# Performance work log

Measured on AMD Instinct MI355X. Metric: run time of the kernel, lower is better.

The kernel has to match this reference:

```python
import jax, jax.numpy as jnp
import numpy as np

TOKEN_ATTEND_SELF_VALUE = -0.0005
LN_EPS = 1e-5


def _layer_norm(x, g, b):
    mu = jnp.mean(x, axis=-1, keepdims=True)
    var = jnp.mean(jnp.square(x - mu), axis=-1, keepdims=True)
    return (x - mu) * jax.lax.rsqrt(var + LN_EPS) * g + b


def _gelu(x):
    return jax.nn.gelu(x, approximate=False)  # torch nn.GELU default is exact erf


def _grouped_ff(x, w1, b1, w2, b2):
    # x: [b, n, L, d]; per-level (grouped conv1d k=1) feedforward
    h = _gelu(jnp.einsum('bnld,ldm->bnlm', x, w1) + b1)
    return _gelu(jnp.einsum('bnlm,lmd->bnld', h, w2) + b2)


def _consensus_attention(levels):
    # levels: [b, n, L, d]; attend_self=False, no local mask
    b, n, L, d = levels.shape
    norm = jnp.maximum(jnp.linalg.norm(levels, axis=-1, keepdims=True), 1e-12)
    k = levels / norm  # F.normalize(dim=-1)
    sim = jnp.einsum('bild,bjld->blij', levels, k) * (d ** -0.5)
    eye = jnp.eye(n, dtype=bool)[None, None, :, :]
    sim = jnp.where(eye, TOKEN_ATTEND_SELF_VALUE, sim)
    attn = jax.nn.softmax(sim, axis=-1)
    return jnp.einsum('blij,bjld->bild', attn, levels)


def setup_inputs() -> dict:
    key = jax.random.key(0)
    ks = jax.random.split(key, 12)
    B, C, H, W = 2, 3, 48, 48
    dim, L = 32, 5
    n = H * W  # sub_patch_size = 1
    s = 0.02
    inp = {
        'img': jax.random.normal(ks[0], (B, C, H, W), jnp.float32),
        'w_tok': jax.random.normal(ks[1], (C, dim), jnp.float32) * s,
        'b_tok': jnp.zeros((dim,), jnp.float32),
        'g_ln_tok': jnp.ones((dim,), jnp.float32),
        'b_ln_tok': jnp.zeros((dim,), jnp.float32),
        'w_lvl': jax.random.normal(ks[2], (C, L * dim), jnp.float32) * s,
        'b_lvl': jnp.zeros((L * dim,), jnp.float32),
        'g_ln_lvl': jnp.ones((dim,), jnp.float32),
        'b_ln_lvl': jnp.zeros((dim,), jnp.float32),
        'pos_emb': jax.random.normal(ks[3], (n, dim), jnp.float32) * s,
        'bu_w1': jax.random.normal(ks[4], (L, dim, 4 * dim), jnp.float32) * s,
        'bu_b1': jnp.zeros((L, 4 * dim), jnp.float32),
        'bu_w2': jax.random.normal(ks[5], (L, 4 * dim, dim), jnp.float32) * s,
        'bu_b2': jnp.zeros((L, dim), jnp.float32),
        'td_w1': jax.random.normal(ks[6], (L - 1, dim, 4 * dim), jnp.float32) * s,
        'td_b1': jnp.zeros((L - 1, 4 * dim), jnp.float32),
        'td_w2': jax.random.normal(ks[7], (L - 1, 4 * dim, dim), jnp.float32) * s,
        'td_b2': jnp.zeros((L - 1, dim), jnp.float32),
        'iters': 3,
    }
    return inp


def reference(img, w_tok, b_tok, g_ln_tok, b_ln_tok, w_lvl, b_lvl, g_ln_lvl,
              b_ln_lvl, pos_emb, bu_w1, bu_b1, bu_w2, bu_b2, td_w1, td_b1,
              td_w2, td_b2, iters):
    B, C, H, W = img.shape
    L = bu_w1.shape[0]
    dim = w_tok.shape[1]
    x = jnp.transpose(img, (0, 2, 3, 1)).reshape(B, H * W, C)  # b n c

    # image_to_tokens: Linear -> LayerNorm -> GELU
    tokens = _gelu(_layer_norm(x @ w_tok + b_tok, g_ln_tok, b_ln_tok))  # [b,n,d]

    # image_to_levels: 1x1 Conv -> GELU -> reshape -> LayerNorm
    lv = _gelu(x @ w_lvl + b_lvl).reshape(B, H * W, L, dim)
    levels = _layer_norm(lv, g_ln_lvl, b_ln_lvl)  # [b,n,L,d]

    pos = pos_emb[None, :, None, :]  # () n () d
    bottom = tokens[:, :, None, :]  # [b,n,1,d]

    num_contrib = jnp.array([4.0] * (L - 1) + [3.0], jnp.float32)[None, None, :, None]

    for _ in range(iters):
        lwi = jnp.concatenate([bottom, levels], axis=2)  # [b,n,L+1,d]
        bu = _grouped_ff(lwi[:, :, :-1, :], bu_w1, bu_b1, bu_w2, bu_b2)
        td = _grouped_ff(lwi[:, :, 2:, :] + pos, td_w1, td_b1, td_w2, td_b2)
        td = jnp.pad(td, ((0, 0), (0, 0), (0, 1), (0, 0)))  # zero at top level
        cons = _consensus_attention(levels)
        levels = (levels + bu + td + cons) / num_contrib

    return levels
```

## Files before the change

kernel.cpp:

```cpp
#include <hip/hip_runtime.h>
#include <math.h>

#define BB 2
#define NN 2304
#define DIM 32
#define LL 5
#define HID 128
#define SJ 8
#define BLN (BB * LL * NN)
#define CONSGRID (SJ * 18 * LL * BB)
#define FFGRID (9 * 36)
#define COMBGRID (BLN / 32)

#define QK_SCALE2 0.25503486f
#define SELF_VAL2 (-7.2134752e-4f)

typedef __attribute__((ext_vector_type(8))) short bf16x8;
typedef __attribute__((ext_vector_type(16))) float f32x16;

union B8U { bf16x8 v; unsigned u[4]; };

__device__ __forceinline__ float b2f(unsigned bits16) {
    union { float f; unsigned u; } c; c.u = bits16 << 16; return c.f;
}
__device__ __forceinline__ unsigned cvt_pk_bf16(float lo, float hi) {
    unsigned r;
    asm("v_cvt_pk_bf16_f32 %0, %1, %2" : "=v"(r) : "v"(lo), "v"(hi));
    return r;
}
__device__ __forceinline__ float gelu_f(float v) {
    return 0.5f * v * (1.0f + erff(v * 0.70710678118654752f));
}
__device__ __forceinline__ void plswap(unsigned a, unsigned b, unsigned& o0, unsigned& o1) {
    auto r = __builtin_amdgcn_permlane32_swap(a, b, false, false);
    o0 = r[0]; o1 = r[1];
}

__global__ __launch_bounds__(256) void prep_all(
    const float* __restrict__ img,
    const float* __restrict__ w_tok, const float* __restrict__ b_tok,
    const float* __restrict__ g_ln_tok, const float* __restrict__ b_ln_tok,
    const float* __restrict__ w_lvl, const float* __restrict__ b_lvl,
    const float* __restrict__ g_ln_lvl, const float* __restrict__ b_ln_lvl,
    const float* __restrict__ pos_emb,
    const float* __restrict__ bu_w1, const float* __restrict__ bu_w2,
    const float* __restrict__ td_w1, const float* __restrict__ td_w2,
    float* __restrict__ levels, short* __restrict__ tokensB,
    short* __restrict__ Qb, short* __restrict__ Ksb, short* __restrict__ Vtb,
    short* __restrict__ TDb, short* __restrict__ W1T, short* __restrict__ W2T)
{
    int blk = blockIdx.x, tid = threadIdx.x;
    int rq = tid >> 2, q = tid & 3, d0 = q * 8;
    if (blk < 72) {
        int t = blk * 64 + rq;
        int b = t / NN, i = t - b * NN;
        float x0 = img[(size_t)(b * 3 + 0) * NN + i];
        float x1 = img[(size_t)(b * 3 + 1) * NN + i];
        float x2 = img[(size_t)(b * 3 + 2) * NN + i];
        float v[8];
        float red = 0.f;
        #pragma unroll
        for (int m = 0; m < 8; ++m) {
            int c = d0 + m;
            v[m] = x0 * w_tok[c] + x1 * w_tok[DIM + c] + x2 * w_tok[2 * DIM + c] + b_tok[c];
            red += v[m];
        }
        red += __shfl_xor(red, 1, 64);
        red += __shfl_xor(red, 2, 64);
        float mu = red * (1.0f / DIM);
        float vr = 0.f;
        #pragma unroll
        for (int m = 0; m < 8; ++m) { float dd = v[m] - mu; vr += dd * dd; }
        vr += __shfl_xor(vr, 1, 64);
        vr += __shfl_xor(vr, 2, 64);
        float rs = rsqrtf(vr * (1.0f / DIM) + 1e-5f);
        unsigned tw[4];
        #pragma unroll
        for (int d2 = 0; d2 < 4; ++d2) {
            int c = d0 + 2 * d2;
            float ya = gelu_f((v[2 * d2] - mu) * rs * g_ln_tok[c] + b_ln_tok[c]);
            float yb = gelu_f((v[2 * d2 + 1] - mu) * rs * g_ln_tok[c + 1] + b_ln_tok[c + 1]);
            tw[d2] = cvt_pk_bf16(ya, yb);
        }
        *(uint4*)(tokensB + (size_t)t * DIM + d0) = make_uint4(tw[0], tw[1], tw[2], tw[3]);
    } else if (blk < 432) {
        int z = blk - 72;
        int b = z / 180, rem = z % 180;
        int l = rem / 36, ic = rem % 36;
        int i = ic * 64 + rq;
        int t = b * NN + i;
        float x0 = img[(size_t)(b * 3 + 0) * NN + i];
        float x1 = img[(size_t)(b * 3 + 1) * NN + i];
        float x2 = img[(size_t)(b * 3 + 2) * NN + i];
        float u[8];
        float red = 0.f;
        #pragma unroll
        for (int m = 0; m < 8; ++m) {
            int c = l * DIM + d0 + m;
            float pre = x0 * w_lvl[c] + x1 * w_lvl[LL * DIM + c] + x2 * w_lvl[2 * LL * DIM + c] + b_lvl[c];
            u[m] = gelu_f(pre);
            red += u[m];
        }
        red += __shfl_xor(red, 1, 64);
        red += __shfl_xor(red, 2, 64);
        float mu = red * (1.0f / DIM);
        float vr = 0.f;
        #pragma unroll
        for (int m = 0; m < 8; ++m) { float dd = u[m] - mu; vr += dd * dd; }
        vr += __shfl_xor(vr, 1, 64);
        vr += __shfl_xor(vr, 2, 64);
        float rs = rsqrtf(vr * (1.0f / DIM) + 1e-5f);
        float y[8];
        float n2p = 0.f;
        #pragma unroll
        for (int m = 0; m < 8; ++m) {
            int c = d0 + m;
            y[m] = (u[m] - mu) * rs * g_ln_lvl[c] + b_ln_lvl[c];
            n2p += y[m] * y[m];
        }
        n2p += __shfl_xor(n2p, 1, 64);
        n2p += __shfl_xor(n2p, 2, 64);
        float ksc = QK_SCALE2 / fmaxf(sqrtf(n2p), 1e-12f);
        size_t lo = ((size_t)t * LL + l) * DIM + d0;
        *(float4*)(levels + lo)     = make_float4(y[0], y[1], y[2], y[3]);
        *(float4*)(levels + lo + 4) = make_float4(y[4], y[5], y[6], y[7]);
        size_t qro = ((size_t)(b * LL + l) * NN + i) * DIM + d0;
        unsigned qw[4], kw[4];
        #pragma unroll
        for (int d2 = 0; d2 < 4; ++d2) {
            qw[d2] = cvt_pk_bf16(y[2 * d2], y[2 * d2 + 1]);
            kw[d2] = cvt_pk_bf16(y[2 * d2] * ksc, y[2 * d2 + 1] * ksc);
        }
        *(uint4*)(Qb + qro)  = make_uint4(qw[0], qw[1], qw[2], qw[3]);
        *(uint4*)(Ksb + qro) = make_uint4(kw[0], kw[1], kw[2], kw[3]);
        #pragma unroll
        for (int d2 = 0; d2 < 4; ++d2) {
            unsigned uv = cvt_pk_bf16(y[2 * d2], y[2 * d2 + 1]);
            Vtb[((size_t)(b * LL + l) * DIM + d0 + 2 * d2) * NN + i]     = (short)uv;
            Vtb[((size_t)(b * LL + l) * DIM + d0 + 2 * d2 + 1) * NN + i] = (short)(uv >> 16);
        }
        if (l >= 1) {
            unsigned dw[4];
            #pragma unroll
            for (int d2 = 0; d2 < 4; ++d2) {
                float p0 = pos_emb[(size_t)i * DIM + d0 + 2 * d2];
                float p1 = pos_emb[(size_t)i * DIM + d0 + 2 * d2 + 1];
                dw[d2] = cvt_pk_bf16(y[2 * d2] + p0, y[2 * d2 + 1] + p1);
            }
            *(uint4*)(TDb + ((size_t)(b * 4 + (l - 1)) * NN + i) * DIM + d0) =
                make_uint4(dw[0], dw[1], dw[2], dw[3]);
        }
    } else {
        int g = blk - 432;
        bool is_bu = g < LL;
        int lw = is_bu ? g : g - LL;
        const float* W1 = (is_bu ? bu_w1 : td_w1) + (size_t)lw * DIM * HID;
        const float* W2 = (is_bu ? bu_w2 : td_w2) + (size_t)lw * HID * DIM;
        short* o1 = W1T + (size_t)g * HID * DIM;
        short* o2 = W2T + (size_t)g * DIM * HID;
        for (int e = tid; e < HID * DIM; e += 256) {
            int m = e >> 5, d = e & 31;
            unsigned u1 = cvt_pk_bf16(W1[(size_t)d * HID + m], 0.f);
            o1[e] = (short)u1;
            int dd = e >> 7, mm = e & 127;
            unsigned u2 = cvt_pk_bf16(W2[(size_t)mm * DIM + dd], 0.f);
            o2[e] = (short)u2;
        }
    }
}

__global__ __launch_bounds__(256) void cons_ff(
    const short* __restrict__ Qb, const short* __restrict__ Ksb,
    const short* __restrict__ Vtb,
    const short* __restrict__ tokensB, const short* __restrict__ TDb,
    const short* __restrict__ W1T, const short* __restrict__ W2T,
    const float* __restrict__ bu_b1, const float* __restrict__ bu_b2,
    const float* __restrict__ td_b1, const float* __restrict__ td_b2,
    short* __restrict__ accp, float* __restrict__ sump,
    float* __restrict__ bu_out, float* __restrict__ td_out)
{
    __shared__ float b1_lds[HID];
    __shared__ float b2_lds[DIM];
    __shared__ __align__(16) float yt_lds[4][DIM * 32];

    int tid = threadIdx.x;
    int w = tid >> 6, lane = tid & 63;
    int li = lane & 31, hi = lane >> 5;

    if (blockIdx.x < CONSGRID) {
        int bid = blockIdx.x;
        int s = bid % SJ; int rest = bid / SJ;
        int ibig = rest % 18; rest /= 18;
        int l = rest % 5, b = rest / 5;
        int i0 = ibig * 128 + w * 32;

        const short* Qrow = Qb + (size_t)(b * LL + l) * NN * DIM;
        const short* Krow = Ksb + (size_t)(b * LL + l) * NN * DIM;
        const short* Vrow = Vtb + (size_t)(b * LL + l) * DIM * NN;

        bf16x8 qf0 = *(const bf16x8*)(Qrow + (size_t)(i0 + li) * DIM + hi * 8);
        bf16x8 qf1 = *(const bf16x8*)(Qrow + (size_t)(i0 + li) * DIM + 16 + hi * 8);

        f32x16 outacc = {};
        float ssum = 0.f;

        for (int jt = 0; jt < NN / SJ / 32; ++jt) {
            int j0 = s * (NN / SJ) + jt * 32;
            bf16x8 kf0 = *(const bf16x8*)(Krow + (size_t)(j0 + li) * DIM + hi * 8);
            bf16x8 kf1 = *(const bf16x8*)(Krow + (size_t)(j0 + li) * DIM + 16 + hi * 8);
            f32x16 st = {};
            st = __builtin_amdgcn_mfma_f32_32x32x16_bf16(kf0, qf0, st, 0, 0, 0);
            st = __builtin_amdgcn_mfma_f32_32x32x16_bf16(kf1, qf1, st, 0, 0, 0);
            float e[16];
            if (j0 == i0) {
                #pragma unroll
                for (int r = 0; r < 16; ++r) {
                    float sc = st[r];
                    if ((((r & 3) + 8 * (r >> 2) + 4 * hi) == li)) sc = SELF_VAL2;
                    e[r] = exp2f(sc);
                }
            } else {
                #pragma unroll
                for (int r = 0; r < 16; ++r) e[r] = exp2f(st[r]);
            }
            #pragma unroll
            for (int r = 0; r < 16; ++r) ssum += e[r];
            unsigned wpk[8];
            #pragma unroll
            for (int h2 = 0; h2 < 8; ++h2)
                wpk[h2] = cvt_pk_bf16(e[2 * h2], e[2 * h2 + 1]);
            B8U pa0, pa1;
            plswap(wpk[0], wpk[2], pa0.u[0], pa0.u[2]);
            plswap(wpk[1], wpk[3], pa0.u[1], pa0.u[3]);
            plswap(wpk[4], wpk[6], pa1.u[0], pa1.u[2]);
            plswap(wpk[5], wpk[7], pa1.u[1], pa1.u[3]);
            bf16x8 vf0 = *(const bf16x8*)(Vrow + (size_t)li * NN + j0 + hi * 8);
            bf16x8 vf1 = *(const bf16x8*)(Vrow + (size_t)li * NN + j0 + 16 + hi * 8);
            outacc = __builtin_amdgcn_mfma_f32_32x32x16_bf16(pa0.v, vf0, outacc, 0, 0, 0);
            outacc = __builtin_amdgcn_mfma_f32_32x32x16_bf16(pa1.v, vf1, outacc, 0, 0, 0);
        }
        size_t base = (size_t)s * BLN + (size_t)(b * LL + l) * NN;
        float ss2 = ssum + __shfl_xor(ssum, 32, 64);
        if (lane < 32) sump[base + i0 + li] = ss2;
        #pragma unroll
        for (int r = 0; r < 16; r += 2) {
            unsigned uo = cvt_pk_bf16(outacc[r], outacc[r + 1]);
            int il = (r & 3) + 8 * (r >> 2) + 4 * hi;
            accp[(base + i0 + il) * DIM + li]     = (short)uo;
            accp[(base + i0 + il + 1) * DIM + li] = (short)(uo >> 16);
        }
    } else {
        int fb = blockIdx.x - CONSGRID;
        int g = fb / 36;
        int tile = fb % 36;

        bool is_bu = g < LL;
        int lw = is_bu ? g : g - LL;
        const float* B1 = (is_bu ? bu_b1 : td_b1) + (size_t)lw * HID;
        const float* B2 = (is_bu ? bu_b2 : td_b2) + (size_t)lw * DIM;
        if (tid < HID) b1_lds[tid] = B1[tid];
        if (tid < DIM) b2_lds[tid] = B2[tid];
        __syncthreads();

        int t0 = tile * 128 + w * 32;
        int b = t0 / NN;
        int i0 = t0 - b * NN;
        const short* xrow =
            (g == 0) ? (tokensB + (size_t)t0 * DIM)
          : is_bu    ? (Qb + ((size_t)(b * LL + (g - 1)) * NN + i0) * DIM)
                     : (TDb + ((size_t)(b * 4 + (g - LL)) * NN + i0) * DIM);
        const short* w1g = W1T + (size_t)g * HID * DIM;
        const short* w2g = W2T + (size_t)g * DIM * HID;

        bf16x8 xb0 = *(const bf16x8*)(xrow + (size_t)li * DIM + hi * 8);
        bf16x8 xb1 = *(const bf16x8*)(xrow + (size_t)li * DIM + 16 + hi * 8);

        f32x16 yacc = {};
        #pragma unroll
        for (int ht = 0; ht < 4; ++ht) {
            bf16x8 a0 = *(const bf16x8*)(w1g + (size_t)(ht * 32 + li) * DIM + hi * 8);
            bf16x8 a1 = *(const bf16x8*)(w1g + (size_t)(ht * 32 + li) * DIM + 16 + hi * 8);
            f32x16 hT = {};
            hT = __builtin_amdgcn_mfma_f32_32x32x16_bf16(a0, xb0, hT, 0, 0, 0);
            hT = __builtin_amdgcn_mfma_f32_32x32x16_bf16(a1, xb1, hT, 0, 0, 0);
            float h[16];
            #pragma unroll
            for (int r = 0; r < 16; ++r) {
                int lrow = (r & 3) + 8 * (r >> 2) + 4 * hi;
                h[r] = gelu_f(hT[r] + b1_lds[ht * 32 + lrow]);
            }
            unsigned wp[8];
            #pragma unroll
            for (int h2 = 0; h2 < 8; ++h2)
                wp[h2] = cvt_pk_bf16(h[2 * h2], h[2 * h2 + 1]);
            B8U hb0, hb1;
            plswap(wp[0], wp[2], hb0.u[0], hb0.u[2]);
            plswap(wp[1], wp[3], hb0.u[1], hb0.u[3]);
            plswap(wp[4], wp[6], hb1.u[0], hb1.u[2]);
            plswap(wp[5], wp[7], hb1.u[1], hb1.u[3]);
            bf16x8 a2 = *(const bf16x8*)(w2g + (size_t)li * HID + ht * 32 + hi * 8);
            bf16x8 a3 = *(const bf16x8*)(w2g + (size_t)li * HID + ht * 32 + 16 + hi * 8);
            yacc = __builtin_amdgcn_mfma_f32_32x32x16_bf16(a2, hb0.v, yacc, 0, 0, 0);
            yacc = __builtin_amdgcn_mfma_f32_32x32x16_bf16(a3, hb1.v, yacc, 0, 0, 0);
        }
        float* yt = yt_lds[w];
        #pragma unroll
        for (int r = 0; r < 16; ++r) {
            int dr = (r & 3) + 8 * (r >> 2) + 4 * hi;
            yt[dr * 32 + li] = gelu_f(yacc[r] + b2_lds[dr]);
        }
        int tk = lane >> 1, dh = (lane & 1) * 16;
        float ov[16];
        #pragma unroll
        for (int j = 0; j < 16; ++j) ov[j] = yt[(dh + j) * 32 + tk];
        float* op = (is_bu ? bu_out : td_out) + ((size_t)(t0 + tk) * LL + lw) * DIM + dh;
        #pragma unroll
        for (int j4 = 0; j4 < 4; ++j4)
            ((float4*)op)[j4] = make_float4(ov[4 * j4], ov[4 * j4 + 1], ov[4 * j4 + 2], ov[4 * j4 + 3]);
    }
}

__global__ __launch_bounds__(256) void combine8(
    const float* __restrict__ levels, const float* __restrict__ bu_buf,
    const float* __restrict__ td_buf, const float* __restrict__ pos_emb,
    const short* __restrict__ accp, const float* __restrict__ sump,
    float* __restrict__ levels_next,
    short* __restrict__ Qb, short* __restrict__ Ksb, short* __restrict__ Vtb,
    short* __restrict__ TDb)
{
    int rw = blockIdx.x * 32 + (threadIdx.x >> 3);
    int dq = threadIdx.x & 7;
    int d0 = dq * 4;
    int b = rw / (LL * NN);
    int l = (rw / NN) % LL;
    int i = rw % NN;
    size_t ro = (size_t)rw;

    float ssum = 0.f;
    #pragma unroll
    for (int s = 0; s < SJ; ++s) ssum += sump[(size_t)s * BLN + ro];
    float inv_s = 1.0f / ssum;
    float nc = (l == LL - 1) ? (1.0f / 3.0f) : 0.25f;

    float ax[4] = {0.f, 0.f, 0.f, 0.f};
    #pragma unroll
    for (int s = 0; s < SJ; ++s) {
        uint2 av = *(const uint2*)(accp + ((size_t)s * BLN + ro) * DIM + d0);
        ax[0] += b2f(av.x & 0xFFFFu);
        ax[1] += b2f(av.x >> 16);
        ax[2] += b2f(av.y & 0xFFFFu);
        ax[3] += b2f(av.y >> 16);
    }

    size_t lo = ((size_t)(b * NN + i) * LL + l) * DIM + d0;
    float4 lv = *(const float4*)(levels + lo);
    float4 bu = *(const float4*)(bu_buf + lo);
    float4 td = (l < LL - 1) ? *(const float4*)(td_buf + lo) : make_float4(0.f, 0.f, 0.f, 0.f);

    float o[4];
    o[0] = (lv.x + bu.x + td.x + ax[0] * inv_s) * nc;
    o[1] = (lv.y + bu.y + td.y + ax[1] * inv_s) * nc;
    o[2] = (lv.z + bu.z + td.z + ax[2] * inv_s) * nc;
    o[3] = (lv.w + bu.w + td.w + ax[3] * inv_s) * nc;
    *(float4*)(levels_next + lo) = make_float4(o[0], o[1], o[2], o[3]);

    float n2p = o[0] * o[0] + o[1] * o[1] + o[2] * o[2] + o[3] * o[3];
    n2p += __shfl_xor(n2p, 1, 64);
    n2p += __shfl_xor(n2p, 2, 64);
    n2p += __shfl_xor(n2p, 4, 64);
    float ksc = QK_SCALE2 / fmaxf(sqrtf(n2p), 1e-12f);

    size_t qro = ro * DIM + d0;
    unsigned q0 = cvt_pk_bf16(o[0], o[1]);
    unsigned q1 = cvt_pk_bf16(o[2], o[3]);
    unsigned k0 = cvt_pk_bf16(o[0] * ksc, o[1] * ksc);
    unsigned k1 = cvt_pk_bf16(o[2] * ksc, o[3] * ksc);
    *(uint2*)(Qb + qro)  = make_uint2(q0, q1);
    *(uint2*)(Ksb + qro) = make_uint2(k0, k1);
    Vtb[((size_t)(b * LL + l) * DIM + d0 + 0) * NN + i] = (short)q0;
    Vtb[((size_t)(b * LL + l) * DIM + d0 + 1) * NN + i] = (short)(q0 >> 16);
    Vtb[((size_t)(b * LL + l) * DIM + d0 + 2) * NN + i] = (short)q1;
    Vtb[((size_t)(b * LL + l) * DIM + d0 + 3) * NN + i] = (short)(q1 >> 16);
    if (l >= 1) {
        float p0 = pos_emb[(size_t)i * DIM + d0 + 0];
        float p1 = pos_emb[(size_t)i * DIM + d0 + 1];
        float p2 = pos_emb[(size_t)i * DIM + d0 + 2];
        float p3 = pos_emb[(size_t)i * DIM + d0 + 3];
        unsigned t0 = cvt_pk_bf16(o[0] + p0, o[1] + p1);
        unsigned t1 = cvt_pk_bf16(o[2] + p2, o[3] + p3);
        *(uint2*)(TDb + ((size_t)(b * 4 + (l - 1)) * NN + i) * DIM + d0) = make_uint2(t0, t1);
    }
}

extern "C" void kernel_launch(void* const* d_in, const int* in_sizes, int n_in,
                              void* d_out, int out_size, void* d_ws, size_t ws_size,
                              hipStream_t stream)
{
    (void)in_sizes; (void)n_in; (void)out_size; (void)ws_size;
    const float* img      = (const float*)d_in[0];
    const float* w_tok    = (const float*)d_in[1];
    const float* b_tok    = (const float*)d_in[2];
    const float* g_ln_tok = (const float*)d_in[3];
    const float* b_ln_tok = (const float*)d_in[4];
    const float* w_lvl    = (const float*)d_in[5];
    const float* b_lvl    = (const float*)d_in[6];
    const float* g_ln_lvl = (const float*)d_in[7];
    const float* b_ln_lvl = (const float*)d_in[8];
    const float* pos_emb  = (const float*)d_in[9];
    const float* bu_w1    = (const float*)d_in[10];
    const float* bu_b1    = (const float*)d_in[11];
    const float* bu_w2    = (const float*)d_in[12];
    const float* bu_b2    = (const float*)d_in[13];
    const float* td_w1    = (const float*)d_in[14];
    const float* td_b1    = (const float*)d_in[15];
    const float* td_w2    = (const float*)d_in[16];
    const float* td_b2    = (const float*)d_in[17];

    float* ws      = (float*)d_ws;
    float* levelsA = ws;
    float* levelsB = levelsA + (size_t)BB * NN * LL * DIM;
    float* bu_buf  = levelsB + (size_t)BB * NN * LL * DIM;
    float* td_buf  = bu_buf  + (size_t)BB * NN * LL * DIM;
    float* sump    = td_buf  + (size_t)BB * NN * LL * DIM;
    short* accp    = (short*)(sump + (size_t)SJ * BLN);
    short* Qb      = accp + (size_t)SJ * BLN * DIM;
    short* Ksb     = Qb   + (size_t)BLN * DIM;
    short* Vtb     = Ksb  + (size_t)BLN * DIM;
    short* tokensB = Vtb  + (size_t)BLN * DIM;
    short* TDb     = tokensB + (size_t)BB * NN * DIM;
    short* W1T     = TDb  + (size_t)BB * 4 * NN * DIM;
    short* W2T     = W1T  + (size_t)9 * HID * DIM;
    float* outp    = (float*)d_out;

    const int cfGrid = CONSGRID + FFGRID;

    prep_all<<<441, 256, 0, stream>>>(
        img, w_tok, b_tok, g_ln_tok, b_ln_tok, w_lvl, b_lvl, g_ln_lvl, b_ln_lvl,
        pos_emb, bu_w1, bu_w2, td_w1, td_w2,
        levelsA, tokensB, Qb, Ksb, Vtb, TDb, W1T, W2T);

    cons_ff<<<cfGrid, 256, 0, stream>>>(Qb, Ksb, Vtb, tokensB, TDb, W1T, W2T,
        bu_b1, bu_b2, td_b1, td_b2, accp, sump, bu_buf, td_buf);
    combine8<<<COMBGRID, 256, 0, stream>>>(levelsA, bu_buf, td_buf, pos_emb,
        accp, sump, levelsB, Qb, Ksb, Vtb, TDb);

    cons_ff<<<cfGrid, 256, 0, stream>>>(Qb, Ksb, Vtb, tokensB, TDb, W1T, W2T,
        bu_b1, bu_b2, td_b1, td_b2, accp, sump, bu_buf, td_buf);
    combine8<<<COMBGRID, 256, 0, stream>>>(levelsB, bu_buf, td_buf, pos_emb,
        accp, sump, levelsA, Qb, Ksb, Vtb, TDb);

    cons_ff<<<cfGrid, 256, 0, stream>>>(Qb, Ksb, Vtb, tokensB, TDb, W1T, W2T,
        bu_b1, bu_b2, td_b1, td_b2, accp, sump, bu_buf, td_buf);
    combine8<<<COMBGRID, 256, 0, stream>>>(levelsA, bu_buf, td_buf, pos_emb,
        accp, sump, outp, Qb, Ksb, Vtb, TDb);
}
```

Before: 125.9 us.

## Drop fp32 levels buffer; store FF outputs in bf16 and reuse Q as levels

```diff
diff --git a/kernel.cpp b/kernel.cpp
--- a/kernel.cpp
+++ b/kernel.cpp
@@ -45,7 +45,7 @@
     const float* __restrict__ pos_emb,
     const float* __restrict__ bu_w1, const float* __restrict__ bu_w2,
     const float* __restrict__ td_w1, const float* __restrict__ td_w2,
-    float* __restrict__ levels, short* __restrict__ tokensB,
+    short* __restrict__ tokensB,
     short* __restrict__ Qb, short* __restrict__ Ksb, short* __restrict__ Vtb,
     short* __restrict__ TDb, short* __restrict__ W1T, short* __restrict__ W2T)
 {
@@ -88,7 +88,6 @@
         int b = z / 180, rem = z % 180;
         int l = rem / 36, ic = rem % 36;
         int i = ic * 64 + rq;
-        int t = b * NN + i;
         float x0 = img[(size_t)(b * 3 + 0) * NN + i];
         float x1 = img[(size_t)(b * 3 + 1) * NN + i];
         float x2 = img[(size_t)(b * 3 + 2) * NN + i];
@@ -121,9 +120,6 @@
         n2p += __shfl_xor(n2p, 1, 64);
         n2p += __shfl_xor(n2p, 2, 64);
         float ksc = QK_SCALE2 / fmaxf(sqrtf(n2p), 1e-12f);
-        size_t lo = ((size_t)t * LL + l) * DIM + d0;
-        *(float4*)(levels + lo)     = make_float4(y[0], y[1], y[2], y[3]);
-        *(float4*)(levels + lo + 4) = make_float4(y[4], y[5], y[6], y[7]);
         size_t qro = ((size_t)(b * LL + l) * NN + i) * DIM + d0;
         unsigned qw[4], kw[4];
         #pragma unroll
@@ -135,9 +131,8 @@
         *(uint4*)(Ksb + qro) = make_uint4(kw[0], kw[1], kw[2], kw[3]);
         #pragma unroll
         for (int d2 = 0; d2 < 4; ++d2) {
-            unsigned uv = cvt_pk_bf16(y[2 * d2], y[2 * d2 + 1]);
-            Vtb[((size_t)(b * LL + l) * DIM + d0 + 2 * d2) * NN + i]     = (short)uv;
-            Vtb[((size_t)(b * LL + l) * DIM + d0 + 2 * d2 + 1) * NN + i] = (short)(uv >> 16);
+            Vtb[((size_t)(b * LL + l) * DIM + d0 + 2 * d2) * NN + i]     = (short)qw[d2];
+            Vtb[((size_t)(b * LL + l) * DIM + d0 + 2 * d2 + 1) * NN + i] = (short)(qw[d2] >> 16);
         }
         if (l >= 1) {
             unsigned dw[4];
@@ -177,7 +172,7 @@
     const float* __restrict__ bu_b1, const float* __restrict__ bu_b2,
     const float* __restrict__ td_b1, const float* __restrict__ td_b2,
     short* __restrict__ accp, float* __restrict__ sump,
-    float* __restrict__ bu_out, float* __restrict__ td_out)
+    short* __restrict__ bu_out, short* __restrict__ td_out)
 {
     __shared__ float b1_lds[HID];
     __shared__ float b2_lds[DIM];
@@ -313,18 +308,20 @@
         float ov[16];
         #pragma unroll
         for (int j = 0; j < 16; ++j) ov[j] = yt[(dh + j) * 32 + tk];
-        float* op = (is_bu ? bu_out : td_out) + ((size_t)(t0 + tk) * LL + lw) * DIM + dh;
-        #pragma unroll
-        for (int j4 = 0; j4 < 4; ++j4)
-            ((float4*)op)[j4] = make_float4(ov[4 * j4], ov[4 * j4 + 1], ov[4 * j4 + 2], ov[4 * j4 + 3]);
+        unsigned up[8];
+        #pragma unroll
+        for (int k = 0; k < 8; ++k) up[k] = cvt_pk_bf16(ov[2 * k], ov[2 * k + 1]);
+        short* op = (is_bu ? bu_out : td_out) + ((size_t)(t0 + tk) * LL + lw) * DIM + dh;
+        *(uint4*)op       = make_uint4(up[0], up[1], up[2], up[3]);
+        *(uint4*)(op + 8) = make_uint4(up[4], up[5], up[6], up[7]);
     }
 }
 
 __global__ __launch_bounds__(256) void combine8(
-    const float* __restrict__ levels, const float* __restrict__ bu_buf,
-    const float* __restrict__ td_buf, const float* __restrict__ pos_emb,
+    const short* __restrict__ bu_buf, const short* __restrict__ td_buf,
+    const float* __restrict__ pos_emb,
     const short* __restrict__ accp, const float* __restrict__ sump,
-    float* __restrict__ levels_next,
+    float* __restrict__ out_f32,
     short* __restrict__ Qb, short* __restrict__ Ksb, short* __restrict__ Vtb,
     short* __restrict__ TDb)
 {
@@ -353,16 +350,26 @@
     }
 
     size_t lo = ((size_t)(b * NN + i) * LL + l) * DIM + d0;
-    float4 lv = *(const float4*)(levels + lo);
-    float4 bu = *(const float4*)(bu_buf + lo);
-    float4 td = (l < LL - 1) ? *(const float4*)(td_buf + lo) : make_float4(0.f, 0.f, 0.f, 0.f);
+    size_t qro = ro * DIM + d0;
+    uint2 lvu = *(const uint2*)(Qb + qro);
+    uint2 buu = *(const uint2*)(bu_buf + lo);
+    float lv0 = b2f(lvu.x & 0xFFFFu), lv1 = b2f(lvu.x >> 16);
+    float lv2 = b2f(lvu.y & 0xFFFFu), lv3 = b2f(lvu.y >> 16);
+    float bu0 = b2f(buu.x & 0xFFFFu), bu1 = b2f(buu.x >> 16);
+    float bu2 = b2f(buu.y & 0xFFFFu), bu3 = b2f(buu.y >> 16);
+    float td0 = 0.f, td1 = 0.f, td2 = 0.f, td3 = 0.f;
+    if (l < LL - 1) {
+        uint2 tdu = *(const uint2*)(td_buf + lo);
+        td0 = b2f(tdu.x & 0xFFFFu); td1 = b2f(tdu.x >> 16);
+        td2 = b2f(tdu.y & 0xFFFFu); td3 = b2f(tdu.y >> 16);
+    }
 
     float o[4];
-    o[0] = (lv.x + bu.x + td.x + ax[0] * inv_s) * nc;
-    o[1] = (lv.y + bu.y + td.y + ax[1] * inv_s) * nc;
-    o[2] = (lv.z + bu.z + td.z + ax[2] * inv_s) * nc;
-    o[3] = (lv.w + bu.w + td.w + ax[3] * inv_s) * nc;
-    *(float4*)(levels_next + lo) = make_float4(o[0], o[1], o[2], o[3]);
+    o[0] = (lv0 + bu0 + td0 + ax[0] * inv_s) * nc;
+    o[1] = (lv1 + bu1 + td1 + ax[1] * inv_s) * nc;
+    o[2] = (lv2 + bu2 + td2 + ax[2] * inv_s) * nc;
+    o[3] = (lv3 + bu3 + td3 + ax[3] * inv_s) * nc;
+    if (out_f32) *(float4*)(out_f32 + lo) = make_float4(o[0], o[1], o[2], o[3]);
 
     float n2p = o[0] * o[0] + o[1] * o[1] + o[2] * o[2] + o[3] * o[3];
     n2p += __shfl_xor(n2p, 1, 64);
@@ -370,7 +377,6 @@
     n2p += __shfl_xor(n2p, 4, 64);
     float ksc = QK_SCALE2 / fmaxf(sqrtf(n2p), 1e-12f);
 
-    size_t qro = ro * DIM + d0;
     unsigned q0 = cvt_pk_bf16(o[0], o[1]);
     unsigned q1 = cvt_pk_bf16(o[2], o[3]);
     unsigned k0 = cvt_pk_bf16(o[0] * ksc, o[1] * ksc);
@@ -416,12 +422,7 @@
     const float* td_w2    = (const float*)d_in[16];
     const float* td_b2    = (const float*)d_in[17];
 
-    float* ws      = (float*)d_ws;
-    float* levelsA = ws;
-    float* levelsB = levelsA + (size_t)BB * NN * LL * DIM;
-    float* bu_buf  = levelsB + (size_t)BB * NN * LL * DIM;
-    float* td_buf  = bu_buf  + (size_t)BB * NN * LL * DIM;
-    float* sump    = td_buf  + (size_t)BB * NN * LL * DIM;
+    float* sump    = (float*)d_ws;
     short* accp    = (short*)(sump + (size_t)SJ * BLN);
     short* Qb      = accp + (size_t)SJ * BLN * DIM;
     short* Ksb     = Qb   + (size_t)BLN * DIM;
@@ -430,6 +431,8 @@
     short* TDb     = tokensB + (size_t)BB * NN * DIM;
     short* W1T     = TDb  + (size_t)BB * 4 * NN * DIM;
     short* W2T     = W1T  + (size_t)9 * HID * DIM;
+    short* bu_buf  = W2T  + (size_t)9 * HID * DIM;
+    short* td_buf  = bu_buf + (size_t)BLN * DIM;
     float* outp    = (float*)d_out;
 
     const int cfGrid = CONSGRID + FFGRID;
@@ -437,20 +440,20 @@
     prep_all<<<441, 256, 0, stream>>>(
         img, w_tok, b_tok, g_ln_tok, b_ln_tok, w_lvl, b_lvl, g_ln_lvl, b_ln_lvl,
         pos_emb, bu_w1, bu_w2, td_w1, td_w2,
-        levelsA, tokensB, Qb, Ksb, Vtb, TDb, W1T, W2T);
+        tokensB, Qb, Ksb, Vtb, TDb, W1T, W2T);
 
     cons_ff<<<cfGrid, 256, 0, stream>>>(Qb, Ksb, Vtb, tokensB, TDb, W1T, W2T,
         bu_b1, bu_b2, td_b1, td_b2, accp, sump, bu_buf, td_buf);
-    combine8<<<COMBGRID, 256, 0, stream>>>(levelsA, bu_buf, td_buf, pos_emb,
-        accp, sump, levelsB, Qb, Ksb, Vtb, TDb);
+    combine8<<<COMBGRID, 256, 0, stream>>>(bu_buf, td_buf, pos_emb,
+        accp, sump, (float*)nullptr, Qb, Ksb, Vtb, TDb);
 
     cons_ff<<<cfGrid, 256, 0, stream>>>(Qb, Ksb, Vtb, tokensB, TDb, W1T, W2T,
         bu_b1, bu_b2, td_b1, td_b2, accp, sump, bu_buf, td_buf);
-    combine8<<<COMBGRID, 256, 0, stream>>>(levelsB, bu_buf, td_buf, pos_emb,
-        accp, sump, levelsA, Qb, Ksb, Vtb, TDb);
+    combine8<<<COMBGRID, 256, 0, stream>>>(bu_buf, td_buf, pos_emb,
+        accp, sump, (float*)nullptr, Qb, Ksb, Vtb, TDb);
 
     cons_ff<<<cfGrid, 256, 0, stream>>>(Qb, Ksb, Vtb, tokensB, TDb, W1T, W2T,
         bu_b1, bu_b2, td_b1, td_b2, accp, sump, bu_buf, td_buf);
-    combine8<<<COMBGRID, 256, 0, stream>>>(levelsA, bu_buf, td_buf, pos_emb,
+    combine8<<<COMBGRID, 256, 0, stream>>>(bu_buf, td_buf, pos_emb,
         accp, sump, outp, Qb, Ksb, Vtb, TDb);
 }
```

After: 123.8 us. About the same (-1.7%).
